# Optimization experiments

Hardware: AMD Instinct MI355X
Metric: run time of the kernel (lower is better)

## Reference

```python
import jax, jax.numpy as jnp
import numpy as np

BETA = 1e-8
ALPHA = 0.5
CHOOSE_K = 128
MEMORY_SIZE = 65536
KEY_DIM = 256
BATCH = 1024


def _l2norm(x, axis=-1, eps=1e-12):
    return x / jnp.sqrt(jnp.sum(x * x, axis=axis, keepdims=True) + eps)


def setup_inputs() -> dict:
    key = jax.random.key(0)
    k1, k2, k3 = jax.random.split(key, 3)
    q = _l2norm(jax.random.normal(k1, (BATCH, KEY_DIM), dtype=jnp.float32))
    memory_key = _l2norm(jax.random.normal(k2, (MEMORY_SIZE, KEY_DIM), dtype=jnp.float32))
    # module init: hist[:] = 1e-5; add small random variation so topk is non-degenerate
    memory_hist = 1e-5 + 1e-3 * jax.random.uniform(k3, (MEMORY_SIZE,), dtype=jnp.float32)
    # module init: values = ones, second half zeroed
    memory_values = jnp.concatenate([
        jnp.ones((MEMORY_SIZE // 2,), dtype=jnp.float32),
        jnp.zeros((MEMORY_SIZE - MEMORY_SIZE // 2,), dtype=jnp.float32),
    ])
    return {"q": q, "memory_key": memory_key,
            "memory_hist": memory_hist, "memory_values": memory_values}


def reference(q, memory_key, memory_hist, memory_values):
    # obtain_topk over FULL memory: dense similarity [B, M]
    sims = jnp.matmul(q, memory_key.T)                      # [B, M]
    scores = jnp.exp(sims - 1.0) * (memory_hist + BETA)[None, :]
    _, k_idxs = jax.lax.top_k(scores, CHOOSE_K)             # [B, K]

    # gather reduced memory at topk indices
    red_keys = memory_key[k_idxs]                           # [B, K, D]
    red_hist = memory_hist[k_idxs] * ALPHA                  # [B, K]
    red_vals = memory_values[k_idxs]                        # [B, K]

    # posterior over the K gathered slots
    sim_k = jnp.einsum('bd,bkd->bk', q, red_keys)           # [B, K]
    joint = jnp.exp(sim_k - 1.0) * (red_hist + BETA)        # [B, K]
    posterior = joint / jnp.sum(joint, axis=1, keepdims=True)
    result = jnp.sum(posterior * red_vals, axis=1)          # [B]
    return result
```

## Files before the change

### kernel.cpp

```cpp
#include <hip/hip_runtime.h>

#define BATCH   1024
#define MSIZE   65536
#define KDIM    256
#define CHOOSEK 128
#define SELK    160
#define BETA    1e-8f
#define ALPHA   0.5f
#define KSC  425.0f
#define KOFF 7.2f

typedef short bf16x8 __attribute__((ext_vector_type(8)));
typedef float f32x4  __attribute__((ext_vector_type(4)));

__device__ inline unsigned int pack2bf(float a, float b) {
    unsigned int ua = __float_as_uint(a);
    unsigned int ub = __float_as_uint(b);
    ua += 0x7fffu + ((ua >> 16) & 1u);
    ub += 0x7fffu + ((ub >> 16) & 1u);
    return (ua >> 16) | (ub & 0xffff0000u);
}

#define GLD16(g, l) __builtin_amdgcn_global_load_lds( \
    (const __attribute__((address_space(1))) unsigned int*)(g), \
    (__attribute__((address_space(3))) unsigned int*)(l), 16, 0, 0)

__global__ __launch_bounds__(256)
void convert_kernel(const float* __restrict__ q, const float* __restrict__ key,
                    const float* __restrict__ hist,
                    unsigned short* __restrict__ qs, unsigned short* __restrict__ kb,
                    float* __restrict__ Ltab)
{
    const int bid = blockIdx.x, tid = threadIdx.x;
    if (bid < 8192) {
        const int off = bid * 256 + tid;
        const float4* s4 = (const float4*)key;
        float4 a = s4[off * 2], b = s4[off * 2 + 1];
        ((uint4*)kb)[off] = make_uint4(pack2bf(a.x, a.y), pack2bf(a.z, a.w),
                                       pack2bf(b.x, b.y), pack2bf(b.z, b.w));
    } else if (bid < 8320) {
        const int f = (bid - 8192) * 256 + tid;
        const int l = f & 63, j = (f >> 6) & 3, ks = (f >> 8) & 7;
        const int wmg = (f >> 11) & 3, bt = (f >> 13) & 3;
        const int r = bt * 256 + wmg * 64 + j * 16 + (l & 15);
        const int c = ks * 32 + (l >> 4) * 8;
        const float* src = q + (size_t)r * KDIM + c;
        float4 a = *(const float4*)src, b = *(const float4*)(src + 4);
        ((uint4*)qs)[f] = make_uint4(pack2bf(a.x, a.y), pack2bf(a.z, a.w),
                                     pack2bf(b.x, b.y), pack2bf(b.z, b.w));
    } else {
        const int n = (bid - 8320) * 256 + tid;
        Ltab[n] = (logf(hist[n] + BETA) + KOFF) * KSC;
    }
}

__global__ __launch_bounds__(512, 4)
void score_kernel(const unsigned short* __restrict__ qs,
                  const unsigned short* __restrict__ kb,
                  const float* __restrict__ Ltab,
                  unsigned char* __restrict__ s8)
{
    __shared__ __align__(16) unsigned short Bs[3][128 * 32];
    const int tid = threadIdx.x;
    const int bid = blockIdx.x;
    const int bt = (bid >> 3) & 3;
    const int b0 = bt * 256;
    const int n0 = ((bid & 7) + ((bid >> 5) << 3)) * 128;
    const int lane = tid & 63, wave = tid >> 6;
    const int wm = (wave >> 1) * 64, wn = (wave & 1) * 64;
    const int l15 = lane & 15, l4 = lane >> 4;
    const int wmg = wave >> 1;

    f32x4 acc[4][4] = {};

    const int srow = tid >> 2;
    const int seg  = (tid & 3) * 8;
    const unsigned short* gB = kb + (size_t)(n0 + srow) * KDIM + seg;
    const int lofs = srow * 32 + seg;

    const bf16x8* qw = (const bf16x8*)qs + (size_t)((bt * 4 + wmg) * 32) * 64 + lane;

    bf16x8 qf[2][4];

#define STAGE_B(st) GLD16(gB + (st) * 32, &Bs[(st) % 3][lofs])

#define STEP(s, WN) do {                                                          \
    asm volatile("s_waitcnt vmcnt(" #WN ")" ::: "memory");                        \
    __builtin_amdgcn_s_barrier();                                                 \
    asm volatile("" ::: "memory");                                                \
    if ((s) < 7) {                                                                \
        _Pragma("unroll")                                                         \
        for (int j = 0; j < 4; ++j)                                               \
            qf[((s) + 1) & 1][j] = qw[(((s) + 1) * 4 + j) * 64];                  \
    }                                                                             \
    if ((s) + 2 < 8) STAGE_B((s) + 2);                                            \
    bf16x8 kf[4];                                                                 \
    _Pragma("unroll")                                                             \
    for (int i = 0; i < 4; ++i)                                                   \
        kf[i] = *(const bf16x8*)(&Bs[(s) % 3][(wn + i * 16 + l15) * 32 + l4 * 8]);\
    __builtin_amdgcn_s_setprio(1);                                                \
    _Pragma("unroll")                                                             \
    for (int i = 0; i < 4; ++i)                                                   \
        _Pragma("unroll")                                                         \
        for (int j = 0; j < 4; ++j)                                               \
            acc[i][j] = __builtin_amdgcn_mfma_f32_16x16x32_bf16(kf[i], qf[(s) & 1][j], acc[i][j], 0, 0, 0); \
    __builtin_amdgcn_s_setprio(0);                                                \
} while (0)

#pragma unroll
    for (int j = 0; j < 4; ++j) qf[0][j] = qw[j * 64];
    STAGE_B(0); STAGE_B(1);

    STEP(0, 1); STEP(1, 1); STEP(2, 1); STEP(3, 1);
    STEP(4, 1); STEP(5, 1); STEP(6, 1); STEP(7, 0);

#undef STEP
#undef STAGE_B

    float4 Lv[4];
#pragma unroll
    for (int i = 0; i < 4; ++i)
        Lv[i] = *(const float4*)&Ltab[n0 + wn + i * 16 + l4 * 4];
#pragma unroll
    for (int j = 0; j < 4; ++j) {
        const size_t row = (size_t)(b0 + wm + j * 16 + l15) * MSIZE;
#pragma unroll
        for (int i = 0; i < 4; ++i) {
            const float* lv = (const float*)&Lv[i];
            unsigned int pk = 0;
#pragma unroll
            for (int reg = 0; reg < 4; ++reg) {
                float x = fmaf(acc[i][j][reg], KSC, lv[reg]);
                x = fminf(fmaxf(x, 0.0f), 255.0f);
                pk |= (unsigned int)(int)x << (8 * reg);
            }
            *(unsigned int*)(s8 + row + (n0 + wn + i * 16 + l4 * 4)) = pk;
        }
    }
}

__global__ __launch_bounds__(256, 4)
void select_kernel(const float* __restrict__ q,
                   const float* __restrict__ key,
                   const float* __restrict__ hist,
                   const float* __restrict__ vals,
                   const unsigned char* __restrict__ s8,
                   float* __restrict__ out)
{
    const int b   = blockIdx.x;
    const int tid = threadIdx.x;

    __shared__ __align__(16) float qs[KDIM];
    __shared__ unsigned int hcnt[16 * 257];
    __shared__ int   stot[256];
    __shared__ int   scal[3];
    __shared__ unsigned short wlist[2048];
    __shared__ int   cidx[1024];
    __shared__ float csc[1024], cjj[1024], cjv[1024];
    __shared__ float wred[8];

    qs[tid] = q[(size_t)b * KDIM + tid];
    const uint4* rowp = reinterpret_cast<const uint4*>(s8 + (size_t)b * MSIZE);
    const unsigned int* roww = reinterpret_cast<const unsigned int*>(rowp);
    const int rep = (tid & 15) * 257;

    int H = -1, nw = 0;
    int minb = 128;
    for (;;) {
        for (int i = tid; i < 16 * 257; i += 256) hcnt[i] = 0u;
        if (tid == 0) { scal[0] = -1; scal[1] = 0; scal[2] = 0; }
        __syncthreads();

        for (int i = 0; i < 16; ++i) {
            uint4 v = rowp[i * 256 + tid];
            unsigned int w[4] = {v.x, v.y, v.z, v.w};
#pragma unroll
            for (int k = 0; k < 4; ++k) {
                if (minb == 0 || (w[k] & 0x80808080u)) {
                    if (minb) {
                        int p = atomicAdd(&scal[2], 1);
                        if (p < 2048) wlist[p] = (unsigned short)((i * 256 + tid) * 4 + k);
                    }
#pragma unroll
                    for (int jj = 0; jj < 4; ++jj) {
                        int bb = (int)((w[k] >> (8 * jj)) & 0xffu);
                        if (bb >= minb) atomicAdd(&hcnt[rep + bb], 1u);
                    }
                }
            }
        }
        __syncthreads();
        { unsigned int t = 0;
#pragma unroll
          for (int k = 0; k < 16; ++k) t += hcnt[k * 257 + tid];
          stot[tid] = (int)t; }
        __syncthreads();

        if (tid < 64) {
            const int l = tid;
            int t0 = stot[l * 4], t1 = stot[l * 4 + 1], t2 = stot[l * 4 + 2], t3 = stot[l * 4 + 3];
            int lsum = t0 + t1 + t2 + t3;
            int s = lsum;
#pragma unroll
            for (int off = 1; off < 64; off <<= 1) {
                int u = __shfl_down(s, off, 64);
                if (l + off < 64) s += u;
            }
            int A  = s - lsum;
            int S3 = A + t3;
            int S2 = S3 + t2;
            int S1 = S2 + t1;
            int S0 = S1 + t0;
            if (S0 >= SELK && S1 < SELK) scal[0] = l * 4 + 0;
            if (S1 >= SELK && S2 < SELK) scal[0] = l * 4 + 1;
            if (S2 >= SELK && S3 < SELK) scal[0] = l * 4 + 2;
            if (S3 >= SELK && A  < SELK) scal[0] = l * 4 + 3;
        }
        __syncthreads();
        H = scal[0]; nw = scal[2];
        __syncthreads();
        if (H >= 0) break;
        minb = 0;
    }

    const unsigned int uH = (unsigned int)H;
    if (minb != 0 && nw <= 2048) {
        for (int i = tid; i < nw; i += 256) {
            const int wi = (int)wlist[i];
            unsigned int w = roww[wi];
#pragma unroll
            for (int jj = 0; jj < 4; ++jj) {
                unsigned int bb = (w >> (8 * jj)) & 0xffu;
                if (bb >= uH) {
                    int p = atomicAdd(&scal[1], 1);
                    if (p < 1024) cidx[p] = wi * 4 + jj;
                }
            }
        }
    } else {
        const bool pre = (H >= 128);
        for (int i = 0; i < 16; ++i) {
            uint4 v = rowp[i * 256 + tid];
            const int base = (i * 256 + tid) * 16;
            unsigned int w[4] = {v.x, v.y, v.z, v.w};
#pragma unroll
            for (int k = 0; k < 4; ++k) {
                if (!pre || (w[k] & 0x80808080u)) {
#pragma unroll
                    for (int jj = 0; jj < 4; ++jj) {
                        unsigned int bb = (w[k] >> (8 * jj)) & 0xffu;
                        if (bb >= uH) {
                            int p = atomicAdd(&scal[1], 1);
                            if (p < 1024) cidx[p] = base + 4 * k + jj;
                        }
                    }
                }
            }
        }
    }
    __syncthreads();
    const int ncand = min(scal[1], 1024);

    const int gid = tid >> 4, gl = tid & 15;
    const float4* q4 = (const float4*)qs;
    for (int i = gid; i < ncand; i += 16) {
        const int idx = cidx[i];
        const float4* kp = (const float4*)(key + (size_t)idx * KDIM);
        float p = 0.f;
#pragma unroll
        for (int u = 0; u < 4; ++u) {
            float4 kk = kp[gl * 4 + u];
            float4 qq = q4[gl * 4 + u];
            p += kk.x * qq.x + kk.y * qq.y + kk.z * qq.z + kk.w * qq.w;
        }
#pragma unroll
        for (int off = 1; off < 16; off <<= 1) p += __shfl_xor(p, off, 64);
        if (gl == 0) {
            float e = expf(p - 1.0f);
            float h = hist[idx];
            csc[i] = e * (h + BETA);
            float j = e * (ALPHA * h + BETA);
            cjj[i] = j;
            cjv[i] = j * vals[idx];
        }
    }
    __syncthreads();

    const int wave = tid >> 6, lane = tid & 63;
    float pn = 0.f, pd = 0.f;
    for (int i = tid; i < ncand; i += 256) {
        float si = csc[i]; int ii = cidx[i]; int rank = 0;
        for (int t = 0; t < ncand; ++t) {
            float st = csc[t];
            rank += (st > si || (st == si && cidx[t] < ii)) ? 1 : 0;
        }
        if (rank < CHOOSEK) { pn += cjv[i]; pd += cjj[i]; }
    }
#pragma unroll
    for (int off = 32; off > 0; off >>= 1) {
        pn += __shfl_xor(pn, off, 64);
        pd += __shfl_xor(pd, off, 64);
    }
    if (lane == 0) { wred[wave] = pn; wred[4 + wave] = pd; }
    __syncthreads();
    if (tid == 0) {
        float n = wred[0] + wred[1] + wred[2] + wred[3];
        float d = wred[4] + wred[5] + wred[6] + wred[7];
        out[b] = n / d;
    }
}

extern "C" void kernel_launch(void* const* d_in, const int* in_sizes, int n_in,
                              void* d_out, int out_size, void* d_ws, size_t ws_size,
                              hipStream_t stream)
{
    (void)in_sizes; (void)n_in; (void)out_size; (void)ws_size;
    const float* q    = (const float*)d_in[0];
    const float* key  = (const float*)d_in[1];
    const float* hist = (const float*)d_in[2];
    const float* vals = (const float*)d_in[3];
    float* out = (float*)d_out;

    unsigned char*  s8 = (unsigned char*)d_ws;
    unsigned short* kb = (unsigned short*)((char*)d_ws + ((size_t)64 << 20));
    unsigned short* qsw= (unsigned short*)((char*)d_ws + ((size_t)96 << 20));
    float*          Lt = (float*)((char*)d_ws + ((size_t)96 << 20) + (512 << 10));

    convert_kernel<<<8576, 256, 0, stream>>>(q, key, hist, qsw, kb, Lt);
    score_kernel<<<2048, 512, 0, stream>>>(qsw, kb, Lt, s8);
    select_kernel<<<BATCH, 256, 0, stream>>>(q, key, hist, vals, s8, out);
}
```

Measured before the change: 210.9 us.

## Emit per-row candidate lists from score kernel to skip full row rescans

The score kernel now appends every quantized score with the high bit set to a per-row global list through a global atomic counter. The list stores the byte value and column index together. The select kernel builds its histogram and candidate set from this compact list instead of scanning the full 64K-byte row, falling back to a full scan if the list overflows or no threshold is found. This removes most of select's row-streaming and histogram atomics, at the cost of global atomics and scattered writes in the score epilogue plus a zeroing block in the convert kernel.

```diff
diff --git a/kernel.cpp b/kernel.cpp
--- a/kernel.cpp
+++ b/kernel.cpp
@@ -5,6 +5,7 @@
 #define KDIM    256
 #define CHOOSEK 128
 #define SELK    160
+#define CAP     4096
 #define BETA    1e-8f
 #define ALPHA   0.5f
 #define KSC  425.0f
@@ -29,7 +30,7 @@
 void convert_kernel(const float* __restrict__ q, const float* __restrict__ key,
                     const float* __restrict__ hist,
                     unsigned short* __restrict__ qs, unsigned short* __restrict__ kb,
-                    float* __restrict__ Ltab)
+                    float* __restrict__ Ltab, unsigned int* __restrict__ gcnt)
 {
     const int bid = blockIdx.x, tid = threadIdx.x;
     if (bid < 8192) {
@@ -48,9 +49,12 @@
         float4 a = *(const float4*)src, b = *(const float4*)(src + 4);
         ((uint4*)qs)[f] = make_uint4(pack2bf(a.x, a.y), pack2bf(a.z, a.w),
                                      pack2bf(b.x, b.y), pack2bf(b.z, b.w));
-    } else {
+    } else if (bid < 8576) {
         const int n = (bid - 8320) * 256 + tid;
         Ltab[n] = (logf(hist[n] + BETA) + KOFF) * KSC;
+    } else {
+        gcnt[tid] = 0u; gcnt[tid + 256] = 0u;
+        gcnt[tid + 512] = 0u; gcnt[tid + 768] = 0u;
     }
 }
 
@@ -58,7 +62,9 @@
 void score_kernel(const unsigned short* __restrict__ qs,
                   const unsigned short* __restrict__ kb,
                   const float* __restrict__ Ltab,
-                  unsigned char* __restrict__ s8)
+                  unsigned char* __restrict__ s8,
+                  unsigned int* __restrict__ gcnt,
+                  unsigned int* __restrict__ glist)
 {
     __shared__ __align__(16) unsigned short Bs[3][128 * 32];
     const int tid = threadIdx.x;
@@ -123,10 +129,12 @@
         Lv[i] = *(const float4*)&Ltab[n0 + wn + i * 16 + l4 * 4];
 #pragma unroll
     for (int j = 0; j < 4; ++j) {
-        const size_t row = (size_t)(b0 + wm + j * 16 + l15) * MSIZE;
+        const int rb = b0 + wm + j * 16 + l15;
+        const size_t row = (size_t)rb * MSIZE;
 #pragma unroll
         for (int i = 0; i < 4; ++i) {
             const float* lv = (const float*)&Lv[i];
+            const int nb = n0 + wn + i * 16 + l4 * 4;
             unsigned int pk = 0;
 #pragma unroll
             for (int reg = 0; reg < 4; ++reg) {
@@ -134,7 +142,23 @@
                 x = fminf(fmaxf(x, 0.0f), 255.0f);
                 pk |= (unsigned int)(int)x << (8 * reg);
             }
-            *(unsigned int*)(s8 + row + (n0 + wn + i * 16 + l4 * 4)) = pk;
+            *(unsigned int*)(s8 + row + nb) = pk;
+            unsigned int m = pk & 0x80808080u;
+            if (m) {
+                int c = __popc(m);
+                unsigned int base = atomicAdd(&gcnt[rb], (unsigned int)c);
+                unsigned int pos = 0;
+#pragma unroll
+                for (int reg = 0; reg < 4; ++reg) {
+                    unsigned int by = (pk >> (8 * reg)) & 0xffu;
+                    if (by & 0x80u) {
+                        unsigned int slot = base + pos;
+                        if (slot < CAP)
+                            glist[(size_t)rb * CAP + slot] = (by << 16) | (unsigned int)(nb + reg);
+                        ++pos;
+                    }
+                }
+            }
         }
     }
 }
@@ -145,6 +169,8 @@
                    const float* __restrict__ hist,
                    const float* __restrict__ vals,
                    const unsigned char* __restrict__ s8,
+                   const unsigned int* __restrict__ gcnt,
+                   const unsigned int* __restrict__ glist,
                    float* __restrict__ out)
 {
     const int b   = blockIdx.x;
@@ -153,39 +179,37 @@
     __shared__ __align__(16) float qs[KDIM];
     __shared__ unsigned int hcnt[16 * 257];
     __shared__ int   stot[256];
-    __shared__ int   scal[3];
-    __shared__ unsigned short wlist[2048];
+    __shared__ int   scal[2];
     __shared__ int   cidx[1024];
     __shared__ float csc[1024], cjj[1024], cjv[1024];
     __shared__ float wred[8];
 
     qs[tid] = q[(size_t)b * KDIM + tid];
     const uint4* rowp = reinterpret_cast<const uint4*>(s8 + (size_t)b * MSIZE);
-    const unsigned int* roww = reinterpret_cast<const unsigned int*>(rowp);
+    const unsigned int* gl = glist + (size_t)b * CAP;
     const int rep = (tid & 15) * 257;
 
-    int H = -1, nw = 0;
-    int minb = 128;
+    const int nl = (int)gcnt[b];
+    int mode = (nl <= CAP) ? 0 : 1;
+
+    int H = -1;
     for (;;) {
         for (int i = tid; i < 16 * 257; i += 256) hcnt[i] = 0u;
-        if (tid == 0) { scal[0] = -1; scal[1] = 0; scal[2] = 0; }
-        __syncthreads();
-
-        for (int i = 0; i < 16; ++i) {
-            uint4 v = rowp[i * 256 + tid];
-            unsigned int w[4] = {v.x, v.y, v.z, v.w};
-#pragma unroll
-            for (int k = 0; k < 4; ++k) {
-                if (minb == 0 || (w[k] & 0x80808080u)) {
-                    if (minb) {
-                        int p = atomicAdd(&scal[2], 1);
-                        if (p < 2048) wlist[p] = (unsigned short)((i * 256 + tid) * 4 + k);
-                    }
-#pragma unroll
-                    for (int jj = 0; jj < 4; ++jj) {
-                        int bb = (int)((w[k] >> (8 * jj)) & 0xffu);
-                        if (bb >= minb) atomicAdd(&hcnt[rep + bb], 1u);
-                    }
+        if (tid == 0) { scal[0] = -1; scal[1] = 0; }
+        __syncthreads();
+
+        if (mode == 0) {
+            for (int i = tid; i < nl; i += 256)
+                atomicAdd(&hcnt[rep + (gl[i] >> 16)], 1u);
+        } else {
+            for (int i = 0; i < 16; ++i) {
+                uint4 v = rowp[i * 256 + tid];
+                unsigned int w[4] = {v.x, v.y, v.z, v.w};
+#pragma unroll
+                for (int k = 0; k < 4; ++k) {
+#pragma unroll
+                    for (int jj = 0; jj < 4; ++jj)
+                        atomicAdd(&hcnt[rep + ((w[k] >> (8 * jj)) & 0xffu)], 1u);
                 }
             }
         }
@@ -217,42 +241,34 @@
             if (S3 >= SELK && A  < SELK) scal[0] = l * 4 + 3;
         }
         __syncthreads();
-        H = scal[0]; nw = scal[2];
+        H = scal[0];
         __syncthreads();
         if (H >= 0) break;
-        minb = 0;
+        mode = 1;
     }
 
     const unsigned int uH = (unsigned int)H;
-    if (minb != 0 && nw <= 2048) {
-        for (int i = tid; i < nw; i += 256) {
-            const int wi = (int)wlist[i];
-            unsigned int w = roww[wi];
-#pragma unroll
-            for (int jj = 0; jj < 4; ++jj) {
-                unsigned int bb = (w >> (8 * jj)) & 0xffu;
-                if (bb >= uH) {
-                    int p = atomicAdd(&scal[1], 1);
-                    if (p < 1024) cidx[p] = wi * 4 + jj;
-                }
+    if (mode == 0) {
+        for (int i = tid; i < nl; i += 256) {
+            unsigned int e = gl[i];
+            if ((e >> 16) >= uH) {
+                int p = atomicAdd(&scal[1], 1);
+                if (p < 1024) cidx[p] = (int)(e & 0xffffu);
             }
         }
     } else {
-        const bool pre = (H >= 128);
         for (int i = 0; i < 16; ++i) {
             uint4 v = rowp[i * 256 + tid];
             const int base = (i * 256 + tid) * 16;
             unsigned int w[4] = {v.x, v.y, v.z, v.w};
 #pragma unroll
             for (int k = 0; k < 4; ++k) {
-                if (!pre || (w[k] & 0x80808080u)) {
-#pragma unroll
-                    for (int jj = 0; jj < 4; ++jj) {
-                        unsigned int bb = (w[k] >> (8 * jj)) & 0xffu;
-                        if (bb >= uH) {
-                            int p = atomicAdd(&scal[1], 1);
-                            if (p < 1024) cidx[p] = base + 4 * k + jj;
-                        }
+#pragma unroll
+                for (int jj = 0; jj < 4; ++jj) {
+                    unsigned int bb = (w[k] >> (8 * jj)) & 0xffu;
+                    if (bb >= uH) {
+                        int p = atomicAdd(&scal[1], 1);
+                        if (p < 1024) cidx[p] = base + 4 * k + jj;
                     }
                 }
             }
@@ -261,7 +277,7 @@
     __syncthreads();
     const int ncand = min(scal[1], 1024);
 
-    const int gid = tid >> 4, gl = tid & 15;
+    const int gid = tid >> 4, gll = tid & 15;
     const float4* q4 = (const float4*)qs;
     for (int i = gid; i < ncand; i += 16) {
         const int idx = cidx[i];
@@ -269,13 +285,13 @@
         float p = 0.f;
 #pragma unroll
         for (int u = 0; u < 4; ++u) {
-            float4 kk = kp[gl * 4 + u];
-            float4 qq = q4[gl * 4 + u];
+            float4 kk = kp[gll * 4 + u];
+            float4 qq = q4[gll * 4 + u];
             p += kk.x * qq.x + kk.y * qq.y + kk.z * qq.z + kk.w * qq.w;
         }
 #pragma unroll
         for (int off = 1; off < 16; off <<= 1) p += __shfl_xor(p, off, 64);
-        if (gl == 0) {
+        if (gll == 0) {
             float e = expf(p - 1.0f);
             float h = hist[idx];
             csc[i] = e * (h + BETA);
@@ -325,8 +341,10 @@
     unsigned short* kb = (unsigned short*)((char*)d_ws + ((size_t)64 << 20));
     unsigned short* qsw= (unsigned short*)((char*)d_ws + ((size_t)96 << 20));
     float*          Lt = (float*)((char*)d_ws + ((size_t)96 << 20) + (512 << 10));
-
-    convert_kernel<<<8576, 256, 0, stream>>>(q, key, hist, qsw, kb, Lt);
-    score_kernel<<<2048, 512, 0, stream>>>(qsw, kb, Lt, s8);
-    select_kernel<<<BATCH, 256, 0, stream>>>(q, key, hist, vals, s8, out);
-}
+    unsigned int* gcnt = (unsigned int*)((char*)d_ws + ((size_t)96 << 20) + (768 << 10));
+    unsigned int* glist= (unsigned int*)((char*)d_ws + ((size_t)97 << 20));
+
+    convert_kernel<<<8577, 256, 0, stream>>>(q, key, hist, qsw, kb, Lt, gcnt);
+    score_kernel<<<2048, 512, 0, stream>>>(qsw, kb, Lt, s8, gcnt, glist);
+    select_kernel<<<BATCH, 256, 0, stream>>>(q, key, hist, vals, s8, gcnt, glist, out);
+}
```

Measured after the change: 297.6 us. +41.1%, slower.
